# Kernel tuning notes

Hardware: AMD Instinct MI355X
Metric: run time of the kernel (lower is better)

Reference implementation:

```python
import jax, jax.numpy as jnp
import numpy as np

N_NODES = 50000
N_EDGES = 800000
IN_CH, HID_CH, OUT_CH = 512, 512, 256


def setup_inputs() -> dict:
    key = jax.random.key(0)
    ks = jax.random.split(key, 8)
    x = jax.random.normal(ks[0], (N_NODES, IN_CH), dtype=jnp.float32)
    edge_index = jax.random.randint(ks[1], (2, N_EDGES), 0, N_NODES, dtype=jnp.int32)
    def glorot(k, fan_in, fan_out):
        s = jnp.sqrt(6.0 / (fan_in + fan_out))
        return jax.random.uniform(k, (fan_in, fan_out), jnp.float32, -s, s)
    W1 = glorot(ks[2], IN_CH, HID_CH)
    b1 = jnp.zeros((HID_CH,), jnp.float32)
    W2 = glorot(ks[3], HID_CH, HID_CH)
    b2 = jnp.zeros((HID_CH,), jnp.float32)
    W3 = glorot(ks[4], HID_CH, OUT_CH)
    b3 = jnp.zeros((OUT_CH,), jnp.float32)
    return {"x": x, "edge_index": edge_index, "W1": W1, "b1": b1,
            "W2": W2, "b2": b2, "W3": W3, "b3": b3}


def _gcn_conv(x, src, dst, W, b, n_nodes):
    """PyG GCNConv: add self-loops, symmetric deg^-1/2 normalization,
    linear transform, scatter-add aggregation, bias."""
    h = x @ W  # [N, out] dense transform first (in >= out)
    # degree counts include the self-loop (+1)
    deg = jax.ops.segment_sum(jnp.ones(src.shape, x.dtype), dst,
                              num_segments=n_nodes) + 1.0
    dinv = jax.lax.rsqrt(deg)  # [N]
    norm = dinv[src] * dinv[dst]  # [E]
    msg = h[src] * norm[:, None]  # [E, out]
    agg = jax.ops.segment_sum(msg, dst, num_segments=n_nodes)
    # self-loop contribution handled analytically: norm_ii = dinv[i]^2
    return agg + h * (dinv * dinv)[:, None] + b


def reference(x, edge_index, W1, b1, W2, b2, W3, b3):
    src, dst = edge_index[0], edge_index[1]
    n = x.shape[0]
    h = _gcn_conv(x, src, dst, W1, b1, n)
    h = jax.nn.gelu(h)  # dropout p=0.0 -> identity
    h = _gcn_conv(h, src, dst, W2, b2, n)
    h = jax.nn.gelu(h)
    out = _gcn_conv(h, src, dst, W3, b3, n)
    return out
```

## Files before the change

### kernel.cpp

```cpp
#include <hip/hip_runtime.h>
#include <hip/hip_fp16.h>
#include <math.h>

#define N_NODES 50000
#define N_EDGES 800000
#define MPAD 50176
#define MT256 (MPAD / 256)
#define KPHYS 1024
#define KB 1024
#define NOUTER 16
#define SCANB ((N_NODES + 255) / 256)


__device__ __forceinline__ unsigned short bf16_rn(float f) {
    unsigned u = __float_as_uint(f);
    u += 0x7FFFu + ((u >> 16) & 1u);
    return (unsigned short)(u >> 16);
}
__device__ __forceinline__ float bf16_f32(unsigned short h) {
    return __uint_as_float(((unsigned)h) << 16);
}

typedef __attribute__((ext_vector_type(2))) float f2v;

__device__ __forceinline__ float2 ntload2(const float* p) {
    f2v v = __builtin_nontemporal_load((const f2v*)p);
    return make_float2(v[0], v[1]);
}


__global__ void zero_int_kernel(int* __restrict__ p, int n) {
    int i = blockIdx.x * blockDim.x + threadIdx.x;
    if (i < n) p[i] = 0;
}

__global__ void count_deg_kernel(const int* __restrict__ dst, int* __restrict__ deg) {
    int e = blockIdx.x * blockDim.x + threadIdx.x;
    if (e < N_EDGES) atomicAdd(&deg[dst[e]], 1);
}

__global__ void dinv_kernel(const int* __restrict__ deg, float* __restrict__ dinv) {
    int i = blockIdx.x * blockDim.x + threadIdx.x;
    if (i < N_NODES) dinv[i] = rsqrtf((float)deg[i] + 1.0f);
}

__global__ __launch_bounds__(256) void scan1_kernel(const int* __restrict__ deg,
                                                    int* __restrict__ local_scan,
                                                    int* __restrict__ partials) {
    __shared__ int sm[256];
    int b = blockIdx.x, t = threadIdx.x;
    int i = b * 256 + t;
    int v = (i < N_NODES) ? deg[i] : 0;
    sm[t] = v;
    __syncthreads();
    for (int off = 1; off < 256; off <<= 1) {
        int x = (t >= off) ? sm[t - off] : 0;
        __syncthreads();
        sm[t] += x;
        __syncthreads();
    }
    if (i < N_NODES) local_scan[i] = sm[t];
    if (t == 255) partials[b] = sm[255];
}

__global__ __launch_bounds__(256) void scan2_kernel(int* __restrict__ partials) {
    __shared__ int sm[256];
    int t = threadIdx.x;
    sm[t] = (t < SCANB) ? partials[t] : 0;
    __syncthreads();
    for (int off = 1; off < 256; off <<= 1) {
        int x = (t >= off) ? sm[t - off] : 0;
        __syncthreads();
        sm[t] += x;
        __syncthreads();
    }
    if (t < SCANB) partials[t] = (t == 0) ? 0 : sm[t - 1];
}

__global__ __launch_bounds__(256) void scan3_kernel(const int* __restrict__ deg,
                                                    const int* __restrict__ local_scan,
                                                    const int* __restrict__ partials,
                                                    int* __restrict__ offsets,
                                                    int* __restrict__ cursor) {
    int i = blockIdx.x * 256 + threadIdx.x;
    if (i == 0) offsets[0] = 0;
    if (i < N_NODES) {
        int incl = local_scan[i] + partials[blockIdx.x];
        offsets[i + 1] = incl;
        cursor[i] = incl - deg[i];
    }
}

__global__ void fill_csr_kernel(const int* __restrict__ src, const int* __restrict__ dst,
                                int* __restrict__ cursor, int2* __restrict__ csr_sw,
                                const float* __restrict__ dinv) {
    int e = blockIdx.x * blockDim.x + threadIdx.x;
    if (e < N_EDGES) {
        int s = src[e], d = dst[e];
        int p = atomicAdd(&cursor[d], 1);
        csr_sw[p] = make_int2(s, __float_as_int(dinv[s] * dinv[d]));
    }
}


typedef __attribute__((ext_vector_type(8))) short bf16x8;
typedef __attribute__((ext_vector_type(4))) float floatx4;

#define GLL16(g, l)                                                                   \
    __builtin_amdgcn_global_load_lds((__attribute__((address_space(1))) const void*)(g), \
                                     (__attribute__((address_space(3))) void*)(l), 16, 0, 0)

__global__ __launch_bounds__(512, 2) void gemm_split_bt(const unsigned short* __restrict__ A2,
                                                        const unsigned short* __restrict__ B2T,
                                                        __half* __restrict__ Chi,
                                                        __half* __restrict__ Clo, int N,
                                                        int cshift) {
    const int b = blockIdx.x;
    const int xcd = b & 7;
    const int q = b >> 3;
    const int cb = q & ((1 << cshift) - 1);
    const int bh = q >> cshift;
    const int r = bh * 8 + xcd;
    if (r >= MT256) return;
    const int row0 = r * 256;
    const int col0 = cb * 256;

    __shared__ unsigned short As[2][2][256 * 32];
    __shared__ unsigned short Bs[2][2][256 * 32];

    const int t = threadIdx.x;
    const int lane = t & 63;
    const int quad = lane >> 4;
    const int l15 = lane & 15;
    const int w = t >> 6;
    const int wm = w >> 2, wn = w & 3;

    floatx4 acc[8][4];
#pragma unroll
    for (int i = 0; i < 8; i++)
#pragma unroll
        for (int j = 0; j < 4; j++) acc[i][j] = (floatx4){0.f, 0.f, 0.f, 0.f};

    const int sr = t >> 2;
    const int sk = ((t & 3) ^ ((t >> 3) & 3)) * 8;
    const unsigned short* Arow0 = A2 + (size_t)(row0 + sr) * KPHYS + sk;
    const unsigned short* Arow1 = Arow0 + (size_t)128 * KPHYS;
    const unsigned short* Brow0 = B2T + (size_t)(col0 + sr) * KB + sk;
    const unsigned short* Brow1 = Brow0 + (size_t)128 * KB;

    const int fcol = (quad ^ ((l15 >> 1) & 3)) * 8;

#define STAGE(buf, k32)                                            \
    do {                                                           \
        GLL16(Arow0 + (k32), As[buf][0] + t * 8);                  \
        GLL16(Arow1 + (k32), As[buf][0] + 4096 + t * 8);           \
        GLL16(Arow0 + 512 + (k32), As[buf][1] + t * 8);            \
        GLL16(Arow1 + 512 + (k32), As[buf][1] + 4096 + t * 8);     \
        GLL16(Brow0 + (k32), Bs[buf][0] + t * 8);                  \
        GLL16(Brow1 + (k32), Bs[buf][0] + 4096 + t * 8);           \
        GLL16(Brow0 + 512 + (k32), Bs[buf][1] + t * 8);            \
        GLL16(Brow1 + 512 + (k32), Bs[buf][1] + 4096 + t * 8);     \
    } while (0)

    STAGE(0, 0);

    for (int it = 0; it < NOUTER; it++) {
        const int cur = it & 1;
        __syncthreads();
        if (it + 1 < NOUTER) STAGE(cur ^ 1, (it + 1) * 32);

        bf16x8 bfh[4], bfl[4];
#pragma unroll
        for (int nt = 0; nt < 4; nt++) {
            const int ro = (wn * 64 + nt * 16 + l15) * 32 + fcol;
            bfh[nt] = *(const bf16x8*)(Bs[cur][0] + ro);
            bfl[nt] = *(const bf16x8*)(Bs[cur][1] + ro);
        }
#pragma unroll
        for (int mt = 0; mt < 8; mt++) {
            const int ro = (wm * 128 + mt * 16 + l15) * 32 + fcol;
            bf16x8 ah = *(const bf16x8*)(As[cur][0] + ro);
            bf16x8 al = *(const bf16x8*)(As[cur][1] + ro);
#pragma unroll
            for (int nt = 0; nt < 4; nt++)
                acc[mt][nt] = __builtin_amdgcn_mfma_f32_16x16x32_bf16(ah, bfh[nt], acc[mt][nt], 0, 0, 0);
#pragma unroll
            for (int nt = 0; nt < 4; nt++)
                acc[mt][nt] = __builtin_amdgcn_mfma_f32_16x16x32_bf16(al, bfh[nt], acc[mt][nt], 0, 0, 0);
#pragma unroll
            for (int nt = 0; nt < 4; nt++)
                acc[mt][nt] = __builtin_amdgcn_mfma_f32_16x16x32_bf16(ah, bfl[nt], acc[mt][nt], 0, 0, 0);
        }
    }
#undef STAGE

#pragma unroll
    for (int mt = 0; mt < 8; mt++) {
#pragma unroll
        for (int rr = 0; rr < 4; rr++) {
            int row = row0 + wm * 128 + mt * 16 + quad * 4 + rr;
            __half* Cph = Chi + (size_t)row * N + col0 + wn * 64 + l15;
            __half* Cpl = Clo + (size_t)row * N + col0 + wn * 64 + l15;
#pragma unroll
            for (int nt = 0; nt < 4; nt++) {
                float a = acc[mt][nt][rr];
                __half hi = __float2half(a);
                __half lo = __float2half(a - __half2float(hi));
                Cph[nt * 16] = hi;
                Cpl[nt * 16] = lo;
            }
        }
    }
}


__global__ void wsplit_kernel(const float* __restrict__ W, unsigned short* __restrict__ B2T, int N) {
    int idx = blockIdx.x * blockDim.x + threadIdx.x;
    if (idx >= 512 * N) return;
    int k = idx / N, n = idx % N;
    float v = W[(size_t)k * N + n];
    unsigned short hi = bf16_rn(v);
    unsigned short lo = bf16_rn(v - bf16_f32(hi));
    unsigned short* row = B2T + (size_t)n * KB;
    row[k] = hi;
    row[512 + k] = lo;
}


__global__ __launch_bounds__(256) void split_x_kernel(const float* __restrict__ x,
                                                      unsigned short* __restrict__ A2) {
    int m = blockIdx.x;
    int ch = threadIdx.x * 2;
    unsigned short* arow = A2 + (size_t)m * KPHYS;
    float vx = 0.f, vy = 0.f;
    if (m < N_NODES) {
        float2 v = ntload2(x + (size_t)m * 512 + ch);
        vx = v.x;
        vy = v.y;
    }
    unsigned short hx = bf16_rn(vx), hy = bf16_rn(vy);
    arow[ch] = hx;
    arow[ch + 1] = hy;
    arow[512 + ch] = bf16_rn(vx - bf16_f32(hx));
    arow[512 + ch + 1] = bf16_rn(vy - bf16_f32(hy));
}


__device__ __forceinline__ float gelu_tanh(float x) {
    float x3 = x * x * x;
    float inner = 0.7978845608028654f * (x + 0.044715f * x3);
    return 0.5f * x * (1.0f + tanhf(inner));
}

__global__ __launch_bounds__(256) void aggregate_split_kernel(
    const __half* __restrict__ Chi, const __half* __restrict__ Clo,
    const int* __restrict__ offsets, const int2* __restrict__ csr_sw,
    const float* __restrict__ dinv,
    const float* __restrict__ bias, unsigned short* __restrict__ A2) {
    int t = threadIdx.x;
    int node = __builtin_amdgcn_readfirstlane(blockIdx.x * 4 + (t >> 6));
    int ch = (t & 63) * 8;
    unsigned short* arow = A2 + (size_t)node * KPHYS;
    if (node >= N_NODES) {
        *(uint4*)(arow + ch) = make_uint4(0, 0, 0, 0);
        *(uint4*)(arow + 512 + ch) = make_uint4(0, 0, 0, 0);
        return;
    }
    int p0 = offsets[node], p1 = offsets[node + 1];
    float a[8] = {0.f, 0.f, 0.f, 0.f, 0.f, 0.f, 0.f, 0.f};

    union H8 { float4 f4; __half2 h2[4]; };
    int p = p0;
    int pend8 = p0 + ((p1 - p0) & ~7);
    for (; p < pend8; p += 8) {
        int2 e[8];
#pragma unroll
        for (int j = 0; j < 8; j++) e[j] = csr_sw[p + j];
        H8 v[8];
#pragma unroll
        for (int j = 0; j < 8; j++)
            v[j].f4 = *(const float4*)(Chi + (size_t)e[j].x * 512 + ch);
#pragma unroll
        for (int j = 0; j < 8; j++) {
            float wg = __int_as_float(e[j].y);
#pragma unroll
            for (int q = 0; q < 4; q++) {
                float2 c = __half22float2(v[j].h2[q]);
                a[2 * q] += wg * c.x;
                a[2 * q + 1] += wg * c.y;
            }
        }
    }
    if (p + 4 <= p1) {
        int2 e[4];
#pragma unroll
        for (int j = 0; j < 4; j++) e[j] = csr_sw[p + j];
        H8 v[4];
#pragma unroll
        for (int j = 0; j < 4; j++)
            v[j].f4 = *(const float4*)(Chi + (size_t)e[j].x * 512 + ch);
#pragma unroll
        for (int j = 0; j < 4; j++) {
            float wg = __int_as_float(e[j].y);
#pragma unroll
            for (int q = 0; q < 4; q++) {
                float2 c = __half22float2(v[j].h2[q]);
                a[2 * q] += wg * c.x;
                a[2 * q + 1] += wg * c.y;
            }
        }
        p += 4;
    }
    for (; p < p1; p++) {
        int2 e = csr_sw[p];
        float wg = __int_as_float(e.y);
        H8 v;
        v.f4 = *(const float4*)(Chi + (size_t)e.x * 512 + ch);
#pragma unroll
        for (int q = 0; q < 4; q++) {
            float2 c = __half22float2(v.h2[q]);
            a[2 * q] += wg * c.x;
            a[2 * q + 1] += wg * c.y;
        }
    }

    float di = dinv[node];
    float wself = di * di;
    H8 vh, vl;
    vh.f4 = *(const float4*)(Chi + (size_t)node * 512 + ch);
    vl.f4 = *(const float4*)(Clo + (size_t)node * 512 + ch);
    float4 bv0 = *(const float4*)(bias + ch);
    float4 bv1 = *(const float4*)(bias + ch + 4);
    float s[8], b[8] = {bv0.x, bv0.y, bv0.z, bv0.w, bv1.x, bv1.y, bv1.z, bv1.w};
#pragma unroll
    for (int j = 0; j < 4; j++) {
        float2 ch2 = __half22float2(vh.h2[j]);
        float2 cl2 = __half22float2(vl.h2[j]);
        s[2 * j] = ch2.x + cl2.x;
        s[2 * j + 1] = ch2.y + cl2.y;
    }

    unsigned short hi[8], lo[8];
#pragma unroll
    for (int j = 0; j < 8; j++) {
        float v = gelu_tanh(a[j] + wself * s[j] + b[j]);
        hi[j] = bf16_rn(v);
        lo[j] = bf16_rn(v - bf16_f32(hi[j]));
    }
    *(ushort4*)(arow + ch) = make_ushort4(hi[0], hi[1], hi[2], hi[3]);
    *(ushort4*)(arow + ch + 4) = make_ushort4(hi[4], hi[5], hi[6], hi[7]);
    *(ushort4*)(arow + 512 + ch) = make_ushort4(lo[0], lo[1], lo[2], lo[3]);
    *(ushort4*)(arow + 512 + ch + 4) = make_ushort4(lo[4], lo[5], lo[6], lo[7]);
}

__global__ __launch_bounds__(256) void aggregate_final_kernel(
    const __half* __restrict__ Chi, const __half* __restrict__ Clo,
    const int* __restrict__ offsets, const int2* __restrict__ csr_sw,
    const float* __restrict__ dinv,
    const float* __restrict__ bias, float* __restrict__ out) {
    int t = threadIdx.x;
    int node = __builtin_amdgcn_readfirstlane(blockIdx.x * 4 + (t >> 6));
    if (node >= N_NODES) return;
    int ch = (t & 63) * 4;
    int p0 = offsets[node], p1 = offsets[node + 1];
    float ax = 0.f, ay = 0.f, az = 0.f, aw = 0.f;

    union H4 { float2 f2; __half2 h2[2]; };
    int p = p0;
    int pend8 = p0 + ((p1 - p0) & ~7);
    for (; p < pend8; p += 8) {
        int2 e[8];
#pragma unroll
        for (int j = 0; j < 8; j++) e[j] = csr_sw[p + j];
        H4 v[8];
#pragma unroll
        for (int j = 0; j < 8; j++)
            v[j].f2 = *(const float2*)(Chi + (size_t)e[j].x * 256 + ch);
#pragma unroll
        for (int j = 0; j < 8; j++) {
            float wg = __int_as_float(e[j].y);
            float2 c0 = __half22float2(v[j].h2[0]), c1 = __half22float2(v[j].h2[1]);
            ax += wg * c0.x; ay += wg * c0.y; az += wg * c1.x; aw += wg * c1.y;
        }
    }
    for (; p < p1; p++) {
        int2 e = csr_sw[p];
        float wg = __int_as_float(e.y);
        H4 v;
        v.f2 = *(const float2*)(Chi + (size_t)e.x * 256 + ch);
        float2 c0 = __half22float2(v.h2[0]), c1 = __half22float2(v.h2[1]);
        ax += wg * c0.x; ay += wg * c0.y; az += wg * c1.x; aw += wg * c1.y;
    }

    float di = dinv[node];
    float wself = di * di;
    H4 vh, vl;
    vh.f2 = *(const float2*)(Chi + (size_t)node * 256 + ch);
    vl.f2 = *(const float2*)(Clo + (size_t)node * 256 + ch);
    float2 h0 = __half22float2(vh.h2[0]), h1 = __half22float2(vh.h2[1]);
    float2 l0 = __half22float2(vl.h2[0]), l1 = __half22float2(vl.h2[1]);
    float4 bv = *(const float4*)(bias + ch);
    float4 o = make_float4(ax + wself * (h0.x + l0.x) + bv.x,
                           ay + wself * (h0.y + l0.y) + bv.y,
                           az + wself * (h1.x + l1.x) + bv.z,
                           aw + wself * (h1.y + l1.y) + bv.w);
    *(float4*)(out + (size_t)node * 256 + ch) = o;
}


static inline char* align16(char* p) { return (char*)(((size_t)p + 15) & ~(size_t)15); }

extern "C" void kernel_launch(void* const* d_in, const int* in_sizes, int n_in,
                              void* d_out, int out_size, void* d_ws, size_t ws_size,
                              hipStream_t stream) {
    const float* x  = (const float*)d_in[0];
    const int* eidx = (const int*)d_in[1];
    const float* W1 = (const float*)d_in[2];
    const float* b1 = (const float*)d_in[3];
    const float* W2 = (const float*)d_in[4];
    const float* b2 = (const float*)d_in[5];
    const float* W3 = (const float*)d_in[6];
    const float* b3 = (const float*)d_in[7];
    float* out = (float*)d_out;

    const int* src = eidx;
    const int* dst = eidx + N_EDGES;

    char* ws = (char*)d_ws;
    unsigned short* A2 = (unsigned short*)ws;  ws += (size_t)MPAD * KPHYS * 2;
    __half* Chi = (__half*)ws;                 ws += (size_t)MPAD * 512 * 2;
    __half* Clo = (__half*)ws;                 ws += (size_t)MPAD * 512 * 2;
    unsigned short* B2T1 = (unsigned short*)ws; ws += (size_t)512 * KB * 2;
    unsigned short* B2T2 = (unsigned short*)ws; ws += (size_t)512 * KB * 2;
    unsigned short* B2T3 = (unsigned short*)ws; ws += (size_t)256 * KB * 2;
    int* deg = (int*)ws;        ws = align16(ws + (size_t)N_NODES * 4);
    float* dinv = (float*)ws;   ws = align16(ws + (size_t)N_NODES * 4);
    int* offsets = (int*)ws;    ws = align16(ws + (size_t)(N_NODES + 1) * 4);
    int* cursor = (int*)ws;     ws = align16(ws + (size_t)N_NODES * 4);
    int2* csr_sw = (int2*)ws;   ws = align16(ws + (size_t)N_EDGES * 8);
    int* local_scan = (int*)ws; ws = align16(ws + (size_t)N_NODES * 4);
    int* partials = (int*)ws;   ws = align16(ws + (size_t)SCANB * 4);

    zero_int_kernel<<<(N_NODES + 255) / 256, 256, 0, stream>>>(deg, N_NODES);
    count_deg_kernel<<<(N_EDGES + 255) / 256, 256, 0, stream>>>(dst, deg);
    dinv_kernel<<<(N_NODES + 255) / 256, 256, 0, stream>>>(deg, dinv);
    scan1_kernel<<<SCANB, 256, 0, stream>>>(deg, local_scan, partials);
    scan2_kernel<<<1, 256, 0, stream>>>(partials);
    scan3_kernel<<<SCANB, 256, 0, stream>>>(deg, local_scan, partials, offsets, cursor);
    fill_csr_kernel<<<(N_EDGES + 255) / 256, 256, 0, stream>>>(src, dst, cursor, csr_sw, dinv);

    wsplit_kernel<<<(512 * 512 + 255) / 256, 256, 0, stream>>>(W1, B2T1, 512);
    wsplit_kernel<<<(512 * 512 + 255) / 256, 256, 0, stream>>>(W2, B2T2, 512);
    wsplit_kernel<<<(512 * 256 + 255) / 256, 256, 0, stream>>>(W3, B2T3, 256);
    split_x_kernel<<<MPAD, 256, 0, stream>>>(x, A2);

    const int gemm_grid_512 = 8 * ((MT256 + 7) / 8) * 2;
    const int gemm_grid_256 = 8 * ((MT256 + 7) / 8) * 1;

    {
        gemm_split_bt<<<gemm_grid_512, 512, 0, stream>>>(A2, B2T1, Chi, Clo, 512, 1);
        aggregate_split_kernel<<<MPAD / 4, 256, 0, stream>>>(Chi, Clo, offsets, csr_sw, dinv, b1, A2);
    }
    {
        gemm_split_bt<<<gemm_grid_512, 512, 0, stream>>>(A2, B2T2, Chi, Clo, 512, 1);
        aggregate_split_kernel<<<MPAD / 4, 256, 0, stream>>>(Chi, Clo, offsets, csr_sw, dinv, b2, A2);
    }
    {
        gemm_split_bt<<<gemm_grid_256, 512, 0, stream>>>(A2, B2T3, Chi, Clo, 256, 0);
        aggregate_final_kernel<<<MPAD / 4, 256, 0, stream>>>(Chi, Clo, offsets, csr_sw, dinv, b3, out);
    }
}
```

Before: 863.0 us.

## Merge dinv into scan3, batch weight splits, use nontemporal loads in aggregation

Folds the dinv computation into scan3 and merges the three weight-split launches into one grid-stride kernel, removing three kernel launches. It also switches the CSR edge reads and the self-row reads in the aggregation kernels to nontemporal loads, so streamed data is less likely to evict the gathered feature rows from cache. The launch savings are only a few microseconds, and the cache-hint effect depends on hardware behaviour.

Result: no change. 861.3 us (-0.2%).

```diff
diff --git a/kernel.cpp b/kernel.cpp
--- a/kernel.cpp
+++ b/kernel.cpp
@@ -22,11 +22,19 @@
 }
 
 typedef __attribute__((ext_vector_type(2))) float f2v;
+typedef __attribute__((ext_vector_type(4))) float f4v;
 
 __device__ __forceinline__ float2 ntload2(const float* p) {
     f2v v = __builtin_nontemporal_load((const f2v*)p);
     return make_float2(v[0], v[1]);
 }
+__device__ __forceinline__ f4v ntload4f(const void* p) {
+    return __builtin_nontemporal_load((const f4v*)p);
+}
+__device__ __forceinline__ int2 ntload_edge(const int2* p) {
+    long long raw = __builtin_nontemporal_load((const long long*)p);
+    return make_int2((int)(raw & 0xffffffffLL), (int)(raw >> 32));
+}
 
 
 __global__ void zero_int_kernel(int* __restrict__ p, int n) {
@@ -37,11 +45,6 @@
 __global__ void count_deg_kernel(const int* __restrict__ dst, int* __restrict__ deg) {
     int e = blockIdx.x * blockDim.x + threadIdx.x;
     if (e < N_EDGES) atomicAdd(&deg[dst[e]], 1);
-}
-
-__global__ void dinv_kernel(const int* __restrict__ deg, float* __restrict__ dinv) {
-    int i = blockIdx.x * blockDim.x + threadIdx.x;
-    if (i < N_NODES) dinv[i] = rsqrtf((float)deg[i] + 1.0f);
 }
 
 __global__ __launch_bounds__(256) void scan1_kernel(const int* __restrict__ deg,
@@ -81,13 +84,16 @@
                                                     const int* __restrict__ local_scan,
                                                     const int* __restrict__ partials,
                                                     int* __restrict__ offsets,
-                                                    int* __restrict__ cursor) {
+                                                    int* __restrict__ cursor,
+                                                    float* __restrict__ dinv) {
     int i = blockIdx.x * 256 + threadIdx.x;
     if (i == 0) offsets[0] = 0;
     if (i < N_NODES) {
+        int d = deg[i];
         int incl = local_scan[i] + partials[blockIdx.x];
         offsets[i + 1] = incl;
-        cursor[i] = incl - deg[i];
+        cursor[i] = incl - d;
+        dinv[i] = rsqrtf((float)d + 1.0f);
     }
 }
 
@@ -214,16 +220,26 @@
 }
 
 
-__global__ void wsplit_kernel(const float* __restrict__ W, unsigned short* __restrict__ B2T, int N) {
-    int idx = blockIdx.x * blockDim.x + threadIdx.x;
-    if (idx >= 512 * N) return;
-    int k = idx / N, n = idx % N;
-    float v = W[(size_t)k * N + n];
-    unsigned short hi = bf16_rn(v);
-    unsigned short lo = bf16_rn(v - bf16_f32(hi));
-    unsigned short* row = B2T + (size_t)n * KB;
-    row[k] = hi;
-    row[512 + k] = lo;
+__global__ void wsplit_all_kernel(const float* __restrict__ W1, unsigned short* __restrict__ B2T1,
+                                  const float* __restrict__ W2, unsigned short* __restrict__ B2T2,
+                                  const float* __restrict__ W3, unsigned short* __restrict__ B2T3) {
+    const int total = 512 * 512 + 512 * 512 + 512 * 256;
+    for (int idx = blockIdx.x * blockDim.x + threadIdx.x; idx < total;
+         idx += gridDim.x * blockDim.x) {
+        const float* W;
+        unsigned short* B2T;
+        int li, N;
+        if (idx < 512 * 512) { W = W1; B2T = B2T1; li = idx; N = 512; }
+        else if (idx < 2 * 512 * 512) { W = W2; B2T = B2T2; li = idx - 512 * 512; N = 512; }
+        else { W = W3; B2T = B2T3; li = idx - 2 * 512 * 512; N = 256; }
+        int k = li / N, n = li % N;
+        float v = W[(size_t)k * N + n];
+        unsigned short hi = bf16_rn(v);
+        unsigned short lo = bf16_rn(v - bf16_f32(hi));
+        unsigned short* row = B2T + (size_t)n * KB;
+        row[k] = hi;
+        row[512 + k] = lo;
+    }
 }
 
 
@@ -269,13 +285,13 @@
     int p0 = offsets[node], p1 = offsets[node + 1];
     float a[8] = {0.f, 0.f, 0.f, 0.f, 0.f, 0.f, 0.f, 0.f};
 
-    union H8 { float4 f4; __half2 h2[4]; };
+    union H8 { float4 f4; f4v v4; __half2 h2[4]; };
     int p = p0;
     int pend8 = p0 + ((p1 - p0) & ~7);
     for (; p < pend8; p += 8) {
         int2 e[8];
 #pragma unroll
-        for (int j = 0; j < 8; j++) e[j] = csr_sw[p + j];
+        for (int j = 0; j < 8; j++) e[j] = ntload_edge(csr_sw + p + j);
         H8 v[8];
 #pragma unroll
         for (int j = 0; j < 8; j++)
@@ -294,7 +310,7 @@
     if (p + 4 <= p1) {
         int2 e[4];
 #pragma unroll
-        for (int j = 0; j < 4; j++) e[j] = csr_sw[p + j];
+        for (int j = 0; j < 4; j++) e[j] = ntload_edge(csr_sw + p + j);
         H8 v[4];
 #pragma unroll
         for (int j = 0; j < 4; j++)
@@ -312,7 +328,7 @@
         p += 4;
     }
     for (; p < p1; p++) {
-        int2 e = csr_sw[p];
+        int2 e = ntload_edge(csr_sw + p);
         float wg = __int_as_float(e.y);
         H8 v;
         v.f4 = *(const float4*)(Chi + (size_t)e.x * 512 + ch);
@@ -327,8 +343,8 @@
     float di = dinv[node];
     float wself = di * di;
     H8 vh, vl;
-    vh.f4 = *(const float4*)(Chi + (size_t)node * 512 + ch);
-    vl.f4 = *(const float4*)(Clo + (size_t)node * 512 + ch);
+    vh.v4 = ntload4f(Chi + (size_t)node * 512 + ch);
+    vl.v4 = ntload4f(Clo + (size_t)node * 512 + ch);
     float4 bv0 = *(const float4*)(bias + ch);
     float4 bv1 = *(const float4*)(bias + ch + 4);
     float s[8], b[8] = {bv0.x, bv0.y, bv0.z, bv0.w, bv1.x, bv1.y, bv1.z, bv1.w};
@@ -365,13 +381,13 @@
     int p0 = offsets[node], p1 = offsets[node + 1];
     float ax = 0.f, ay = 0.f, az = 0.f, aw = 0.f;
 
-    union H4 { float2 f2; __half2 h2[2]; };
+    union H4 { float2 f2; f2v v2; __half2 h2[2]; };
     int p = p0;
     int pend8 = p0 + ((p1 - p0) & ~7);
     for (; p < pend8; p += 8) {
         int2 e[8];
 #pragma unroll
-        for (int j = 0; j < 8; j++) e[j] = csr_sw[p + j];
+        for (int j = 0; j < 8; j++) e[j] = ntload_edge(csr_sw + p + j);
         H4 v[8];
 #pragma unroll
         for (int j = 0; j < 8; j++)
@@ -384,7 +400,7 @@
         }
     }
     for (; p < p1; p++) {
-        int2 e = csr_sw[p];
+        int2 e = ntload_edge(csr_sw + p);
         float wg = __int_as_float(e.y);
         H4 v;
         v.f2 = *(const float2*)(Chi + (size_t)e.x * 256 + ch);
@@ -395,8 +411,8 @@
     float di = dinv[node];
     float wself = di * di;
     H4 vh, vl;
-    vh.f2 = *(const float2*)(Chi + (size_t)node * 256 + ch);
-    vl.f2 = *(const float2*)(Clo + (size_t)node * 256 + ch);
+    vh.v2 = __builtin_nontemporal_load((const f2v*)(Chi + (size_t)node * 256 + ch));
+    vl.v2 = __builtin_nontemporal_load((const f2v*)(Clo + (size_t)node * 256 + ch));
     float2 h0 = __half22float2(vh.h2[0]), h1 = __half22float2(vh.h2[1]);
     float2 l0 = __half22float2(vl.h2[0]), l1 = __half22float2(vl.h2[1]);
     float4 bv = *(const float4*)(bias + ch);
@@ -443,15 +459,12 @@
 
     zero_int_kernel<<<(N_NODES + 255) / 256, 256, 0, stream>>>(deg, N_NODES);
     count_deg_kernel<<<(N_EDGES + 255) / 256, 256, 0, stream>>>(dst, deg);
-    dinv_kernel<<<(N_NODES + 255) / 256, 256, 0, stream>>>(deg, dinv);
     scan1_kernel<<<SCANB, 256, 0, stream>>>(deg, local_scan, partials);
     scan2_kernel<<<1, 256, 0, stream>>>(partials);
-    scan3_kernel<<<SCANB, 256, 0, stream>>>(deg, local_scan, partials, offsets, cursor);
+    scan3_kernel<<<SCANB, 256, 0, stream>>>(deg, local_scan, partials, offsets, cursor, dinv);
     fill_csr_kernel<<<(N_EDGES + 255) / 256, 256, 0, stream>>>(src, dst, cursor, csr_sw, dinv);
 
-    wsplit_kernel<<<(512 * 512 + 255) / 256, 256, 0, stream>>>(W1, B2T1, 512);
-    wsplit_kernel<<<(512 * 512 + 255) / 256, 256, 0, stream>>>(W2, B2T2, 512);
-    wsplit_kernel<<<(512 * 256 + 255) / 256, 256, 0, stream>>>(W3, B2T3, 256);
+    wsplit_all_kernel<<<640, 256, 0, stream>>>(W1, B2T1, W2, B2T2, W3, B2T3);
     split_x_kernel<<<MPAD, 256, 0, stream>>>(x, A2);
 
     const int gemm_grid_512 = 8 * ((MT256 + 7) / 8) * 2;
```
